# Kernel tuning notes

Hardware: AMD Instinct MI355X
Metric: run time of the kernel (lower is better)

## Reference

```python
import jax, jax.numpy as jnp
import numpy as np

B, D, H, N, K, C = 1024, 256, 512, 100000, 96, 10


def setup_inputs() -> dict:
    key = jax.random.key(0)
    ks = jax.random.split(key, 16)
    s = 0.02
    return {
        "x": jax.random.normal(ks[0], (B, D), jnp.float32),
        "candidate_x": jax.random.normal(ks[1], (N, D), jnp.float32),
        "candidate_labels": jax.random.randint(ks[2], (N,), 0, C, jnp.int32),
        "W_enc": jax.random.normal(ks[3], (D, H), jnp.float32) * s,
        "b_enc": jnp.zeros((H,), jnp.float32),
        "W_key": jax.random.normal(ks[4], (H, H), jnp.float32) * s,
        "b_key": jnp.zeros((H,), jnp.float32),
        "W_val": jax.random.normal(ks[5], (H, H), jnp.float32) * s,
        "b_val": jnp.zeros((H,), jnp.float32),
        "E_label": jax.random.normal(ks[6], (C, H), jnp.float32) * s,
        "W_t1": jax.random.normal(ks[7], (H, H), jnp.float32) * s,
        "b_t1": jnp.zeros((H,), jnp.float32),
        "W_t2": jax.random.normal(ks[8], (H, H), jnp.float32) * s,
    }


def reference(x, candidate_x, candidate_labels, W_enc, b_enc, W_key, b_key,
              W_val, b_val, E_label, W_t1, b_t1, W_t2):
    # Encode queries and candidates
    x_enc = x @ W_enc + b_enc                       # [B, H]
    cand_enc = candidate_x @ W_enc + b_enc          # [N, H]
    x_key = x_enc @ W_key + b_key                   # [B, H]
    cand_keys = cand_enc @ W_key + b_key            # [N, H]

    # Negative euclidean distance via GEMM expansion (compute-efficient cdist)
    q2 = jnp.sum(x_key * x_key, axis=-1, keepdims=True)        # [B, 1]
    c2 = jnp.sum(cand_keys * cand_keys, axis=-1)               # [N]
    d2 = q2 + c2[None, :] - 2.0 * (x_key @ cand_keys.T)        # [B, N]
    sim = -jnp.sqrt(jnp.maximum(d2, 0.0))                      # [B, N]

    # Top-k retrieval
    top_sims, top_idx = jax.lax.top_k(sim, K)                  # [B, K]

    cand_vals = cand_enc @ W_val + b_val                       # [N, H]
    label_emb = E_label[candidate_labels]                      # [N, H]

    ctx_keys = cand_keys[top_idx]                              # [B, K, H]
    ctx_labels = label_emb[top_idx]                            # [B, K, H]
    _ = cand_vals[top_idx]  # gathered values (unused by the original math)

    # Attention over retrieved context (softmax of top-k similarities)
    attn = jax.nn.softmax(top_sims, axis=1)                    # [B, K]

    # Correction MLP T (dropout is identity in eval mode)
    diff = x_key[:, None, :] - ctx_keys                        # [B, K, H]
    t_out = jax.nn.relu(diff @ W_t1 + b_t1) @ W_t2             # [B, K, H]

    ctx_vec = jnp.sum(attn[..., None] * (ctx_labels + t_out), axis=1)  # [B, H]
    return x_enc + ctx_vec
```

## Files before the change

kernel.cpp:

```cpp
#include <hip/hip_runtime.h>
#include <cfloat>
#include <cmath>

#define B_ 1024
#define D_ 256
#define H_ 512
#define N_ 100000
#define K_ 96
#define C_ 10
#define SAMP 4096
#define CAPC 4096
#define RCAP 15

typedef __attribute__((ext_vector_type(8))) short bf16x8;
typedef __attribute__((ext_vector_type(4))) float f32x4;

__device__ __forceinline__ float bf2f(ushort h) {
    union { unsigned u; float f; } v; v.u = ((unsigned)h) << 16; return v.f;
}
__device__ __forceinline__ ushort f2bf(float f) {
    union { float f; unsigned u; } v; v.f = f;
    unsigned u = v.u;
    unsigned r = (u + 0x7fffu + ((u >> 16) & 1u)) >> 16;
    return (ushort)r;
}
__device__ __forceinline__ unsigned f2key(float f) {
    unsigned u = __float_as_uint(f);
    return (u & 0x80000000u) ? ~u : (u | 0x80000000u);
}
__device__ __forceinline__ float d2_of(float acc, float q2, float c2) {
    return fmaxf(fmaf(-2.f, acc, q2 + c2), 0.f);
}

#define GLDS(g, l)                                                            \
    __builtin_amdgcn_global_load_lds(                                         \
        (const __attribute__((address_space(1))) void*)(g),                   \
        (__attribute__((address_space(3))) void*)(l), 16, 0, 0)

#define FENCE() asm volatile("" ::: "memory")

template <int RELU>
__global__ __launch_bounds__(256) void gemm_nn(const float* __restrict__ A,
                                               const float* __restrict__ Bm,
                                               const float* __restrict__ bias,
                                               float* __restrict__ Cm,
                                               int M, int N, int Kd) {
    __shared__ float sA[16][68];
    __shared__ float sB[16][64];
    const int t  = threadIdx.x;
    const int tx = t & 15, ty = t >> 4;
    const int m0 = blockIdx.y * 64;
    const int n0 = blockIdx.x * 64;
    const int lr = t >> 2;
    const int lk = (t & 3) << 2;
    const int bk = t >> 4;
    const int bn = (t & 15) << 2;

    float acc[4][4] = {};
    for (int k0 = 0; k0 < Kd; k0 += 16) {
        float4 av = make_float4(0.f, 0.f, 0.f, 0.f);
        if (m0 + lr < M)
            av = *(const float4*)(A + (size_t)(m0 + lr) * Kd + k0 + lk);
        sA[lk + 0][lr] = av.x; sA[lk + 1][lr] = av.y;
        sA[lk + 2][lr] = av.z; sA[lk + 3][lr] = av.w;
        float4 bv = *(const float4*)(Bm + (size_t)(k0 + bk) * N + n0 + bn);
        *(float4*)&sB[bk][bn] = bv;
        __syncthreads();
#pragma unroll
        for (int kk = 0; kk < 16; ++kk) {
            float4 a4 = *(const float4*)&sA[kk][ty << 2];
            float4 b4 = *(const float4*)&sB[kk][tx << 2];
            float ar[4] = {a4.x, a4.y, a4.z, a4.w};
            float br[4] = {b4.x, b4.y, b4.z, b4.w};
#pragma unroll
            for (int i = 0; i < 4; ++i)
#pragma unroll
                for (int j = 0; j < 4; ++j)
                    acc[i][j] = fmaf(ar[i], br[j], acc[i][j]);
        }
        __syncthreads();
    }
#pragma unroll
    for (int i = 0; i < 4; ++i) {
        int row = m0 + (ty << 2) + i;
        if (row < M) {
            int col = n0 + (tx << 2);
            float b0 = 0.f, b1 = 0.f, b2 = 0.f, b3 = 0.f;
            if (bias) { b0 = bias[col]; b1 = bias[col + 1]; b2 = bias[col + 2]; b3 = bias[col + 3]; }
            float4 o;
            o.x = acc[i][0] + b0; o.y = acc[i][1] + b1;
            o.z = acc[i][2] + b2; o.w = acc[i][3] + b3;
            if (RELU) {
                o.x = fmaxf(o.x, 0.f); o.y = fmaxf(o.y, 0.f);
                o.z = fmaxf(o.z, 0.f); o.w = fmaxf(o.w, 0.f);
            }
            *(float4*)(Cm + (size_t)row * N + col) = o;
        }
    }
}

template <int MODE, int SWZ>
__global__ __launch_bounds__(256) void gemm_nt(const ushort* __restrict__ A,
                                               const ushort* __restrict__ Bv,
                                               const float* __restrict__ bias,
                                               const float* __restrict__ q2v,
                                               const float* __restrict__ c2v,
                                               const float* __restrict__ thrv,
                                               float* __restrict__ candV,
                                               int* __restrict__ candI,
                                               int* __restrict__ cnt,
                                               void* __restrict__ Cout,
                                               int M, int Nlim, int K,
                                               int ldc, int nvalid, int per) {
    int m0, n0;
    if (SWZ == 0) {
        m0 = blockIdx.y * 128; n0 = blockIdx.x * 128;
    } else if (SWZ == 1) {
        int bid = blockIdx.x;
        int xcd = bid & 7, slot = bid >> 3;
        m0 = (slot & 7) * 128;
        n0 = (xcd * per + (slot >> 3)) * 128;
        if (n0 >= nvalid || m0 >= M) return;
    } else {
        int bid = blockIdx.x;
        int xcd = bid & 7, slot = bid >> 3;
        n0 = (slot & 3) * 128;
        m0 = (xcd * per + (slot >> 2)) * 128;
        if (m0 >= M) return;
    }

    __shared__ __align__(16) char smem[32768];
    const int t = threadIdx.x;
    const int lane = t & 63, w = t >> 6;
    const int wm = w & 1, wn = w >> 1;

    f32x4 acc[4][4];
#pragma unroll
    for (int i = 0; i < 4; ++i)
#pragma unroll
        for (int j = 0; j < 4; ++j)
            acc[i][j] = (f32x4){0.f, 0.f, 0.f, 0.f};

    const int la = lane & 15, lk = lane >> 4;
    const int aoff = (wm * 64 + la) * 64 + lk * 16;
    const int boff = (wn * 64 + la) * 64 + lk * 16;
    const int r_ = t >> 2, cc_ = (t & 3);

    auto stage = [&](int k0, int buf) {
#pragma unroll
        for (int q = 0; q < 2; ++q) {
            int r = r_ + q * 64;
            int ar = m0 + r; ar = (ar < M) ? ar : (M - 1);
            GLDS(A + (size_t)ar * K + k0 + cc_ * 8,
                 (char*)smem + buf * 8192 + (q * 256 + t) * 16);
            int br = n0 + r; br = (br < Nlim) ? br : (Nlim - 1);
            GLDS(Bv + (size_t)br * K + k0 + cc_ * 8,
                 (char*)smem + 16384 + buf * 8192 + (q * 256 + t) * 16);
        }
    };

    stage(0, 0);
    int cur = 0;
    for (int k0 = 0; k0 < K; k0 += 32) {
        if (k0 + 32 < K) {
            stage(k0 + 32, cur ^ 1);
            FENCE();
            asm volatile("s_waitcnt vmcnt(4)" ::: "memory");
        } else {
            FENCE();
            asm volatile("s_waitcnt vmcnt(0)" ::: "memory");
        }
        __builtin_amdgcn_s_barrier(); FENCE();

        bf16x8 af[4], bfr[4];
        const char* pA = (const char*)smem + cur * 8192 + aoff;
        const char* pB = (const char*)smem + 16384 + cur * 8192 + boff;
#pragma unroll
        for (int i = 0; i < 4; ++i)
            af[i] = *(const bf16x8*)(pA + i * 1024);
#pragma unroll
        for (int j = 0; j < 4; ++j)
            bfr[j] = *(const bf16x8*)(pB + j * 1024);
#pragma unroll
        for (int i = 0; i < 4; ++i)
#pragma unroll
            for (int j = 0; j < 4; ++j)
                acc[i][j] = __builtin_amdgcn_mfma_f32_16x16x32_bf16(
                    af[i], bfr[j], acc[i][j], 0, 0, 0);

        FENCE();
        asm volatile("s_waitcnt lgkmcnt(0)" ::: "memory");
        __builtin_amdgcn_s_barrier(); FENCE();
        cur ^= 1;
    }

    const int rl = (lane >> 4) * 4, cl = lane & 15;

    if (MODE == 7) {
#pragma unroll
        for (int i = 0; i < 4; ++i) {
#pragma unroll
            for (int v = 0; v < 4; ++v) {
                int gr = m0 + wm * 64 + i * 16 + rl + v;
                float s = 0.f;
#pragma unroll
                for (int j = 0; j < 4; ++j) {
                    int gc = n0 + wn * 64 + j * 16 + cl;
                    float val = acc[i][j][v] + bias[gc];
                    float vb = bf2f(f2bf(val));
                    s = fmaf(vb, vb, s);
                }
                s += __shfl_xor(s, 1);
                s += __shfl_xor(s, 2);
                s += __shfl_xor(s, 4);
                s += __shfl_xor(s, 8);
                if (cl == 0 && gr < M) atomicAdd(&candV[gr], s);
            }
        }
        return;
    }

    if (MODE == 5) {
        float* stV = (float*)smem;
        int*   stI = (int*)(smem + 7680);
        int*   stC = (int*)(smem + 15360);
        for (int r = t; r < 128; r += 256) stC[r] = 0;
        __syncthreads();
#pragma unroll
        for (int i = 0; i < 4; ++i) {
#pragma unroll
            for (int v = 0; v < 4; ++v) {
                int rloc = wm * 64 + i * 16 + rl + v;
                int gr = m0 + rloc;
                float q2b = q2v[gr];
                float th = thrv[gr];
#pragma unroll
                for (int j = 0; j < 4; ++j) {
                    int gc = n0 + wn * 64 + j * 16 + cl;
                    if (gc < nvalid) {
                        float d2 = d2_of(acc[i][j][v], q2b, c2v[gc]);
                        if (d2 <= th) {
                            int p = atomicAdd(&stC[rloc], 1);
                            if (p < RCAP) {
                                stV[rloc * RCAP + p] = d2;
                                stI[rloc * RCAP + p] = gc;
                            } else {
                                int gp = atomicAdd(&cnt[gr], 1);
                                if (gp < CAPC) {
                                    candV[(size_t)gr * CAPC + gp] = d2;
                                    candI[(size_t)gr * CAPC + gp] = gc;
                                }
                            }
                        }
                    }
                }
            }
        }
        __syncthreads();
        for (int r = t; r < 128; r += 256) {
            int n = stC[r]; if (n > RCAP) n = RCAP;
            if (n > 0) {
                int gr = m0 + r;
                int gb = atomicAdd(&cnt[gr], n);
                for (int q = 0; q < n; ++q) {
                    int pos = gb + q;
                    if (pos < CAPC) {
                        candV[(size_t)gr * CAPC + pos] = stV[r * RCAP + q];
                        candI[(size_t)gr * CAPC + pos] = stI[r * RCAP + q];
                    }
                }
            }
        }
        return;
    }

#pragma unroll
    for (int i = 0; i < 4; ++i) {
#pragma unroll
        for (int j = 0; j < 4; ++j) {
            int gc = n0 + wn * 64 + j * 16 + cl;
#pragma unroll
            for (int v = 0; v < 4; ++v) {
                int gr = m0 + wm * 64 + i * 16 + rl + v;
                if (gr < M && gc < nvalid) {
                    float val = acc[i][j][v];
                    if (MODE == 2) {
                        ((float*)Cout)[(size_t)gr * ldc + gc] = val;
                    } else if (MODE == 4) {
                        ((float*)Cout)[(size_t)gr * ldc + gc] = val + bias[gc];
                    } else {
                        if (MODE == 3) val += bias[gc];
                        ((ushort*)Cout)[(size_t)gr * ldc + gc] = f2bf(val);
                    }
                }
            }
        }
    }
}

__global__ __launch_bounds__(256) void thr_select(const float* __restrict__ S,
                                                  int ld,
                                                  const float* __restrict__ q2v,
                                                  const float* __restrict__ c2v,
                                                  float* __restrict__ thrArr) {
    __shared__ unsigned keys[SAMP];
    __shared__ int hist[256];
    __shared__ int sel[2];
    const int b = blockIdx.x, t = threadIdx.x;
    const float q2b = q2v[b];
    for (int i = t; i < SAMP; i += 256)
        keys[i] = ~f2key(d2_of(S[(size_t)b * ld + i], q2b, c2v[i]));
    __syncthreads();
    unsigned prefix = 0, mask = 0;
    int rank = K_;
    for (int shift = 24; shift >= 0; shift -= 8) {
        hist[t & 255] = 0;
        __syncthreads();
        for (int i = t; i < SAMP; i += 256) {
            unsigned k = keys[i];
            if ((k & mask) == prefix) atomicAdd(&hist[(k >> shift) & 255], 1);
        }
        __syncthreads();
        if (t == 0) {
            int r = rank, d = 255;
            for (; d > 0; --d) { int c = hist[d]; if (r - c <= 0) break; r -= c; }
            sel[0] = d; sel[1] = (r < 1) ? 1 : r;
        }
        __syncthreads();
        prefix |= ((unsigned)sel[0]) << shift;
        rank = sel[1];
        mask |= (0xFFu << shift);
        __syncthreads();
    }
    if (t == 0) {
        unsigned key = ~prefix;
        thrArr[b] = __uint_as_float(key & 0x7FFFFFFFu);
    }
}

__global__ __launch_bounds__(256) void final_select(const float* __restrict__ candV,
                                                    const int* __restrict__ candI,
                                                    const int* __restrict__ cnt,
                                                    float* __restrict__ topV,
                                                    int* __restrict__ topI) {
    __shared__ unsigned keys[CAPC];
    __shared__ int hist[256];
    __shared__ int sel[2];
    __shared__ int poscnt, eqcnt;
    const int b = blockIdx.x, t = threadIdx.x;
    int n = cnt[b]; if (n > CAPC) n = CAPC;
    for (int i = t; i < n; i += 256)
        keys[i] = ~f2key(candV[(size_t)b * CAPC + i]);
    __syncthreads();
    unsigned prefix = 0, mask = 0;
    int rank = K_;
    for (int shift = 24; shift >= 0; shift -= 8) {
        hist[t & 255] = 0;
        __syncthreads();
        for (int i = t; i < n; i += 256) {
            unsigned k = keys[i];
            if ((k & mask) == prefix) atomicAdd(&hist[(k >> shift) & 255], 1);
        }
        __syncthreads();
        if (t == 0) {
            int r = rank, d = 255;
            for (; d > 0; --d) { int c = hist[d]; if (r - c <= 0) break; r -= c; }
            sel[0] = d; sel[1] = (r < 1) ? 1 : r;
        }
        __syncthreads();
        prefix |= ((unsigned)sel[0]) << shift;
        rank = sel[1];
        mask |= (0xFFu << shift);
        __syncthreads();
    }
    unsigned kth = prefix;
    if (t == 0) { poscnt = 0; eqcnt = 0; }
    __syncthreads();
    for (int i = t; i < n; i += 256) {
        if (keys[i] > kth) {
            int p = atomicAdd(&poscnt, 1);
            topV[b * K_ + p] = candV[(size_t)b * CAPC + i];
            topI[b * K_ + p] = candI[(size_t)b * CAPC + i];
        }
    }
    __syncthreads();
    int base = poscnt;
    for (int i = t; i < n; i += 256) {
        if (keys[i] == kth) {
            int p = atomicAdd(&eqcnt, 1);
            if (base + p < K_) {
                topV[b * K_ + base + p] = candV[(size_t)b * CAPC + i];
                topI[b * K_ + base + p] = candI[(size_t)b * CAPC + i];
            }
        }
    }
}

__global__ void init_cnt(int* cnt) {
    int i = blockIdx.x * 256 + threadIdx.x;
    if (i < B_) cnt[i] = 0;
}

__global__ void init_f32(float* p, int n) {
    int i = blockIdx.x * 256 + threadIdx.x;
    int stride = gridDim.x * 256;
    for (; i < n; i += stride) p[i] = 0.f;
}

__global__ void conv_f2b(const float* __restrict__ in, ushort* __restrict__ out, int n) {
    int i = (blockIdx.x * 256 + threadIdx.x) * 4;
    int stride = gridDim.x * 256 * 4;
    for (; i < n; i += stride) {
        float4 v = *(const float4*)(in + i);
        ushort4 o;
        o.x = f2bf(v.x); o.y = f2bf(v.y); o.z = f2bf(v.z); o.w = f2bf(v.w);
        *(ushort4*)(out + i) = o;
    }
}

__global__ void conv_f2b_s(const float* __restrict__ in, ushort* __restrict__ out,
                           int ldin) {
    int i = (blockIdx.x * 256 + threadIdx.x) * 4;
    int stride = gridDim.x * 256 * 4;
    int total = B_ * H_;
    for (; i < total; i += stride) {
        int r = i >> 9, c = i & 511;
        float4 v = *(const float4*)(in + (size_t)r * ldin + c);
        ushort4 o;
        o.x = f2bf(v.x); o.y = f2bf(v.y); o.z = f2bf(v.z); o.w = f2bf(v.w);
        *(ushort4*)(out + i) = o;
    }
}

__global__ __launch_bounds__(256) void transpose_f2b(const float* __restrict__ in,
                                                     ushort* __restrict__ out,
                                                     int R, int Cn) {
    __shared__ float tile[32][33];
    int bx = blockIdx.x * 32, by = blockIdx.y * 32;
    int tx = threadIdx.x & 31, ty = threadIdx.x >> 5;
    int x = bx + tx;
#pragma unroll
    for (int dy = 0; dy < 32; dy += 8) {
        int y = by + ty + dy;
        if (x < Cn && y < R) tile[ty + dy][tx] = in[(size_t)y * Cn + x];
    }
    __syncthreads();
    int ox = by + tx;
#pragma unroll
    for (int dy = 0; dy < 32; dy += 8) {
        int oy = bx + ty + dy;
        if (ox < R && oy < Cn) out[(size_t)oy * R + ox] = f2bf(tile[tx][ty + dy]);
    }
}

__global__ void pack_wxx(const float* __restrict__ W_enc,
                         const float* __restrict__ Wc,
                         const float* __restrict__ b_enc,
                         const float* __restrict__ bc,
                         float* __restrict__ Wxx, float* __restrict__ bxx) {
    int i = blockIdx.x * 256 + threadIdx.x;
    if (i < D_ * H_) {
        int k = i >> 9, h = i & 511;
        Wxx[(size_t)k * 1024 + h] = W_enc[i];
        Wxx[(size_t)k * 1024 + 512 + h] = Wc[i];
    }
    if (i < H_) { bxx[i] = b_enc[i]; bxx[512 + i] = bc[i]; }
}

__global__ __launch_bounds__(64) void q2x_k(const ushort* __restrict__ Xb,
                                            const float* __restrict__ Xf,
                                            int ldx,
                                            const float* __restrict__ bc,
                                            float* __restrict__ outv) {
    const int r = blockIdx.x, t = threadIdx.x;
    const ushort* p  = Xb + (size_t)r * H_ + t * 8;
    const float*  xf = Xf + (size_t)r * ldx + t * 8;
    float nrm = 0.f, dot = 0.f;
#pragma unroll
    for (int j = 0; j < 8; ++j) {
        float v = bf2f(p[j]);
        nrm = fmaf(v, v, nrm);
        dot = fmaf(xf[j], bc[t * 8 + j], dot);
    }
    for (int off = 32; off > 0; off >>= 1) {
        nrm += __shfl_down(nrm, off);
        dot += __shfl_down(dot, off);
    }
    if (t == 0) outv[r] = nrm - 2.f * dot;
}

__global__ void bcomb_k(const float* __restrict__ b_enc,
                        const float* __restrict__ W_key,
                        const float* __restrict__ b_key,
                        float* __restrict__ b_comb) {
    int h = blockIdx.x * 256 + threadIdx.x;
    if (h >= H_) return;
    float acc = b_key[h];
    for (int m = 0; m < H_; ++m)
        acc = fmaf(b_enc[m], W_key[(size_t)m * H_ + h], acc);
    b_comb[h] = acc;
}

__global__ void bq_k(const float* __restrict__ bc,
                     const float* __restrict__ W1,
                     float* __restrict__ bq) {
    int h = blockIdx.x * 256 + threadIdx.x;
    if (h >= H_) return;
    float acc = 0.f;
    for (int m = 0; m < H_; ++m)
        acc = fmaf(bc[m], W1[(size_t)m * H_ + h], acc);
    bq[h] = acc;
}

__global__ __launch_bounds__(128) void softmax_k(const float* __restrict__ topVal,
                                                 float* __restrict__ attn) {
    __shared__ float red[128];
    const int b = blockIdx.x, t = threadIdx.x;
    float v = (t < K_) ? -sqrtf(topVal[b * K_ + t]) : -FLT_MAX;
    red[t] = v; __syncthreads();
    for (int s = 64; s > 0; s >>= 1) {
        if (t < s) red[t] = fmaxf(red[t], red[t + s]);
        __syncthreads();
    }
    float m = red[0]; __syncthreads();
    float e = (t < K_) ? expf(v - m) : 0.f;
    red[t] = e; __syncthreads();
    for (int s = 64; s > 0; s >>= 1) {
        if (t < s) red[t] += red[t + s];
        __syncthreads();
    }
    float ssum = red[0];
    if (t < K_) attn[b * K_ + t] = e / ssum;
}

__global__ __launch_bounds__(256) void wsum_q(const float* __restrict__ attn,
                                              const int* __restrict__ topI,
                                              const float* __restrict__ P,
                                              const ushort* __restrict__ Q,
                                              ushort* __restrict__ hw) {
    __shared__ float aw[K_];
    __shared__ int ai[K_];
    const int b = blockIdx.x, t = threadIdx.x;
    if (t < K_) { aw[t] = attn[b * K_ + t]; ai[t] = topI[b * K_ + t]; }
    __syncthreads();
    const float p0 = P[(size_t)b * H_ + 2 * t];
    const float p1 = P[(size_t)b * H_ + 2 * t + 1];
    float a0 = 0.f, a1 = 0.f;
    for (int k = 0; k < K_; ++k) {
        float w = aw[k];
        ushort2 q = *(const ushort2*)(Q + (size_t)ai[k] * H_ + 2 * t);
        a0 = fmaf(w, fmaxf(p0 - bf2f(q.x), 0.f), a0);
        a1 = fmaf(w, fmaxf(p1 - bf2f(q.y), 0.f), a1);
    }
    ushort2 o; o.x = f2bf(a0); o.y = f2bf(a1);
    *(ushort2*)(hw + (size_t)b * H_ + 2 * t) = o;
}

__global__ __launch_bounds__(256) void final_out(const float* __restrict__ attn,
                                                 const int* __restrict__ topI,
                                                 const int* __restrict__ labels,
                                                 const float* __restrict__ E,
                                                 const float* __restrict__ tsum,
                                                 const float* __restrict__ xe,
                                                 int ldxe,
                                                 float* __restrict__ out) {
    const int b = blockIdx.x, t = threadIdx.x;
    float a0 = 0.f, a1 = 0.f;
    for (int k = 0; k < K_; ++k) {
        float w = attn[b * K_ + k];
        int idx = topI[b * K_ + k];
        int lab = labels[idx];
        const float* el = E + (size_t)lab * H_;
        a0 = fmaf(w, el[t], a0);
        a1 = fmaf(w, el[t + 256], a1);
    }
    out[(size_t)b * H_ + t] =
        xe[(size_t)b * ldxe + t] + a0 + tsum[(size_t)b * H_ + t];
    out[(size_t)b * H_ + t + 256] =
        xe[(size_t)b * ldxe + t + 256] + a1 + tsum[(size_t)b * H_ + t + 256];
}

extern "C" void kernel_launch(void* const* d_in, const int* in_sizes, int n_in,
                              void* d_out, int out_size, void* d_ws, size_t ws_size,
                              hipStream_t stream) {
    const float* x      = (const float*)d_in[0];
    const float* cx     = (const float*)d_in[1];
    const int*   labels = (const int*)d_in[2];
    const float* W_enc  = (const float*)d_in[3];
    const float* b_enc  = (const float*)d_in[4];
    const float* W_key  = (const float*)d_in[5];
    const float* b_key  = (const float*)d_in[6];
    const float* E_label = (const float*)d_in[9];
    const float* W_t1   = (const float*)d_in[10];
    const float* b_t1   = (const float*)d_in[11];
    const float* W_t2   = (const float*)d_in[12];
    float* out = (float*)d_out;

    char* base = (char*)d_ws;
    size_t off = 0;
    auto take = [&](size_t n) -> char* {
        char* p = base + off;
        off = (off + n + 255) & ~(size_t)255;
        return p;
    };
    float*  Wc    = (float*)take((size_t)D_ * H_ * 4);
    float*  bc    = (float*)take((size_t)H_ * 4);
    float*  Wxx   = (float*)take((size_t)D_ * 1024 * 4);
    float*  bxx   = (float*)take((size_t)1024 * 4);
    ushort* WcT   = (ushort*)take((size_t)H_ * D_ * 2);
    ushort* Wcb   = (ushort*)take((size_t)D_ * H_ * 2);
    float*  Wq    = (float*)take((size_t)D_ * H_ * 4);
    ushort* WqT   = (ushort*)take((size_t)H_ * D_ * 2);
    float*  bq    = (float*)take((size_t)H_ * 4);
    ushort* Wt1T  = (ushort*)take((size_t)H_ * H_ * 2);
    ushort* Wt2T  = (ushort*)take((size_t)H_ * H_ * 2);
    float*  xekk  = (float*)take((size_t)B_ * 1024 * 4);
    ushort* xkb   = (ushort*)take((size_t)B_ * H_ * 2);
    ushort* xprojb= (ushort*)take((size_t)B_ * D_ * 2);
    float*  q2x   = (float*)take((size_t)B_ * 4);
    float*  c2    = (float*)take((size_t)N_ * 4);
    float*  topV  = (float*)take((size_t)B_ * K_ * 4);
    int*    topI  = (int*)take((size_t)B_ * K_ * 4);
    float*  thr   = (float*)take((size_t)B_ * 4);
    float*  attn  = (float*)take((size_t)B_ * K_ * 4);
    int*    cnt   = (int*)take((size_t)B_ * 4);
    float*  candV = (float*)take((size_t)B_ * CAPC * 4);
    int*    candI = (int*)take((size_t)B_ * CAPC * 4);
    ushort* hwAll = (ushort*)take((size_t)B_ * H_ * 2);
    float*  tsum  = (float*)take((size_t)B_ * H_ * 4);
    float*  Pbuf  = (float*)take((size_t)B_ * H_ * 4);
    ushort* Qb    = (ushort*)take((size_t)N_ * H_ * 2);
    char*   big   = base + off;

    ushort* cxb = (ushort*)big;
    float* simSmall = (float*)candV;

    const float* xeView = xekk;
    const float* xkView = xekk + 512;

    {
        dim3 g(H_ / 64, D_ / 64);
        gemm_nn<0><<<g, 256, 0, stream>>>(W_enc, W_key, nullptr, Wc, D_, H_, H_);
        bcomb_k<<<(H_ + 255) / 256, 256, 0, stream>>>(b_enc, W_key, b_key, bc);
        gemm_nn<0><<<g, 256, 0, stream>>>(Wc, W_t1, nullptr, Wq, D_, H_, H_);
        bq_k<<<(H_ + 255) / 256, 256, 0, stream>>>(bc, W_t1, bq);
        pack_wxx<<<(D_ * H_ + 255) / 256, 256, 0, stream>>>(W_enc, Wc, b_enc,
                                                            bc, Wxx, bxx);
        dim3 gt1((H_ + 31) / 32, (D_ + 31) / 32);
        transpose_f2b<<<gt1, 256, 0, stream>>>(Wc, WcT, D_, H_);
        transpose_f2b<<<gt1, 256, 0, stream>>>(Wq, WqT, D_, H_);
        conv_f2b<<<128, 256, 0, stream>>>(Wc, Wcb, D_ * H_);
        dim3 gt2((H_ + 31) / 32, (H_ + 31) / 32);
        transpose_f2b<<<gt2, 256, 0, stream>>>(W_t1, Wt1T, H_, H_);
        transpose_f2b<<<gt2, 256, 0, stream>>>(W_t2, Wt2T, H_, H_);
    }
    {
        dim3 gx(1024 / 64, B_ / 64);
        gemm_nn<0><<<gx, 256, 0, stream>>>(x, Wxx, bxx, xekk, B_, 1024, D_);
        conv_f2b_s<<<1024, 256, 0, stream>>>(xkView, xkb, 1024);
        conv_f2b<<<2048, 256, 0, stream>>>(cx, cxb, N_ * D_);
        dim3 gp(D_ / 128, B_ / 128);
        gemm_nt<0, 0><<<gp, 256, 0, stream>>>(
            xkb, Wcb, nullptr, nullptr, nullptr, nullptr, nullptr, nullptr,
            nullptr, xprojb, B_, D_, H_, D_, D_, 0);
        q2x_k<<<B_, 64, 0, stream>>>(xkb, xkView, 1024, bc, q2x);
        dim3 gq(H_ / 128, B_ / 128);
        gemm_nt<4, 0><<<gq, 256, 0, stream>>>(
            xkb, Wt1T, b_t1, nullptr, nullptr, nullptr, nullptr, nullptr,
            nullptr, Pbuf, B_, H_, H_, H_, H_, 0);
    }
    init_f32<<<128, 256, 0, stream>>>(c2, N_);
    {
        int mt = (N_ + 127) / 128;
        int mper = (mt + 7) / 8;
        gemm_nt<7, 2><<<8 * mper * 4, 256, 0, stream>>>(
            cxb, WcT, bc, nullptr, nullptr, nullptr, c2, nullptr, nullptr,
            nullptr, N_, H_, D_, H_, H_, mper);
    }
    {
        int nper = (SAMP / 128 + 7) / 8;
        gemm_nt<2, 1><<<64 * nper, 256, 0, stream>>>(
            xprojb, cxb, nullptr, nullptr, nullptr, nullptr, nullptr, nullptr,
            nullptr, simSmall, B_, N_, D_, SAMP, SAMP, nper);
        thr_select<<<B_, 256, 0, stream>>>(simSmall, SAMP, q2x, c2, thr);
    }
    init_cnt<<<(B_ + 255) / 256, 256, 0, stream>>>(cnt);
    {
        int NT = (N_ + 127) / 128;
        int nper = (NT + 7) / 8;
        gemm_nt<5, 1><<<64 * nper, 256, 0, stream>>>(
            xprojb, cxb, nullptr, q2x, c2, thr, candV, candI, cnt,
            nullptr, B_, N_, D_, 0, N_, nper);
    }
    {
        int mt = (N_ + 127) / 128;
        int mper = (mt + 7) / 8;
        gemm_nt<3, 2><<<8 * mper * 4, 256, 0, stream>>>(
            cxb, WqT, bq, nullptr, nullptr, nullptr, nullptr, nullptr,
            nullptr, Qb, N_, H_, D_, H_, H_, mper);
    }
    final_select<<<B_, 256, 0, stream>>>(candV, candI, cnt, topV, topI);
    softmax_k<<<B_, 128, 0, stream>>>(topV, attn);

    wsum_q<<<B_, 256, 0, stream>>>(attn, topI, Pbuf, Qb, hwAll);
    {
        dim3 g(H_ / 128, B_ / 128);
        gemm_nt<2, 0><<<g, 256, 0, stream>>>(
            hwAll, Wt2T, nullptr, nullptr, nullptr, nullptr, nullptr, nullptr,
            nullptr, tsum, B_, H_, H_, H_, H_, 0);
    }
    final_out<<<B_, 256, 0, stream>>>(attn, topI, labels, E_label, tsum,
                                      xeView, 1024, out);
}
```

Before: 827.0 us.

## Fold query-side projections into one widened packed GEMM from x

The query-side GEMMs (xkb·Wc for xproj, xkb·Wt1 for P) are precomputed as weight products (Wq, G2 = Wc·Wcᵀ) and appended as extra columns to the packed encoder weight, so one GEMM on x yields x_enc, x_key, P and xproj. This removes two dependent GEMM launches, the bf16 conversion of x_key, and the Pbuf buffer. It adds a small Wc·Wcᵀ GEMM and a wider main GEMM, and rounding changes because the products now go through fp32 weight folding instead of bf16 activations.

Result: no change. 837.8 us (+1.3%).

```diff
diff --git a/kernel.cpp b/kernel.cpp
--- a/kernel.cpp
+++ b/kernel.cpp
@@ -11,6 +11,7 @@
 #define SAMP 4096
 #define CAPC 4096
 #define RCAP 15
+#define WXN 1792
 
 typedef __attribute__((ext_vector_type(8))) short bf16x8;
 typedef __attribute__((ext_vector_type(4))) float f32x4;
@@ -286,8 +287,6 @@
                     float val = acc[i][j][v];
                     if (MODE == 2) {
                         ((float*)Cout)[(size_t)gr * ldc + gc] = val;
-                    } else if (MODE == 4) {
-                        ((float*)Cout)[(size_t)gr * ldc + gc] = val + bias[gc];
                     } else {
                         if (MODE == 3) val += bias[gc];
                         ((ushort*)Cout)[(size_t)gr * ldc + gc] = f2bf(val);
@@ -418,13 +417,13 @@
     }
 }
 
-__global__ void conv_f2b_s(const float* __restrict__ in, ushort* __restrict__ out,
-                           int ldin) {
+__global__ void conv_rows(const float* __restrict__ in, ushort* __restrict__ out,
+                          int R, int C, int ldin) {
     int i = (blockIdx.x * 256 + threadIdx.x) * 4;
     int stride = gridDim.x * 256 * 4;
-    int total = B_ * H_;
+    int total = R * C;
     for (; i < total; i += stride) {
-        int r = i >> 9, c = i & 511;
+        int r = i / C, c = i % C;
         float4 v = *(const float4*)(in + (size_t)r * ldin + c);
         ushort4 o;
         o.x = f2bf(v.x); o.y = f2bf(v.y); o.z = f2bf(v.z); o.w = f2bf(v.w);
@@ -455,32 +454,48 @@
 
 __global__ void pack_wxx(const float* __restrict__ W_enc,
                          const float* __restrict__ Wc,
+                         const float* __restrict__ Wq,
+                         const float* __restrict__ G2,
                          const float* __restrict__ b_enc,
                          const float* __restrict__ bc,
+                         const float* __restrict__ bq,
+                         const float* __restrict__ b_t1,
+                         const float* __restrict__ bcw,
                          float* __restrict__ Wxx, float* __restrict__ bxx) {
     int i = blockIdx.x * 256 + threadIdx.x;
-    if (i < D_ * H_) {
-        int k = i >> 9, h = i & 511;
-        Wxx[(size_t)k * 1024 + h] = W_enc[i];
-        Wxx[(size_t)k * 1024 + 512 + h] = Wc[i];
-    }
-    if (i < H_) { bxx[i] = b_enc[i]; bxx[512 + i] = bc[i]; }
-}
-
-__global__ __launch_bounds__(64) void q2x_k(const ushort* __restrict__ Xb,
-                                            const float* __restrict__ Xf,
+    int total = D_ * WXN;
+    if (i < total) {
+        int k = i / WXN, c = i % WXN;
+        float v;
+        if (c < 512)       v = W_enc[(size_t)k * 512 + c];
+        else if (c < 1024) v = Wc[(size_t)k * 512 + (c - 512)];
+        else if (c < 1536) v = Wq[(size_t)k * 512 + (c - 1024)];
+        else               v = G2[(size_t)k * 256 + (c - 1536)];
+        Wxx[(size_t)k * WXN + c] = v;
+    }
+    if (i < WXN) {
+        float b;
+        if (i < 512)       b = b_enc[i];
+        else if (i < 1024) b = bc[i - 512];
+        else if (i < 1536) b = bq[i - 1024] + b_t1[i - 1024];
+        else               b = bcw[i - 1536];
+        bxx[i] = b;
+    }
+}
+
+__global__ __launch_bounds__(64) void q2x_k(const float* __restrict__ Xf,
                                             int ldx,
                                             const float* __restrict__ bc,
                                             float* __restrict__ outv) {
     const int r = blockIdx.x, t = threadIdx.x;
-    const ushort* p  = Xb + (size_t)r * H_ + t * 8;
-    const float*  xf = Xf + (size_t)r * ldx + t * 8;
+    const float* xf = Xf + (size_t)r * ldx + t * 8;
     float nrm = 0.f, dot = 0.f;
 #pragma unroll
     for (int j = 0; j < 8; ++j) {
-        float v = bf2f(p[j]);
+        float raw = xf[j];
+        float v = bf2f(f2bf(raw));
         nrm = fmaf(v, v, nrm);
-        dot = fmaf(xf[j], bc[t * 8 + j], dot);
+        dot = fmaf(raw, bc[t * 8 + j], dot);
     }
     for (int off = 32; off > 0; off >>= 1) {
         nrm += __shfl_down(nrm, off);
@@ -512,6 +527,17 @@
     bq[h] = acc;
 }
 
+__global__ void bcw_k(const float* __restrict__ bc,
+                      const float* __restrict__ Wc,
+                      float* __restrict__ outv) {
+    int d = blockIdx.x * 256 + threadIdx.x;
+    if (d >= D_) return;
+    float acc = 0.f;
+    for (int h = 0; h < H_; ++h)
+        acc = fmaf(bc[h], Wc[(size_t)d * H_ + h], acc);
+    outv[d] = acc;
+}
+
 __global__ __launch_bounds__(128) void softmax_k(const float* __restrict__ topVal,
                                                  float* __restrict__ attn) {
     __shared__ float red[128];
@@ -536,6 +562,7 @@
 __global__ __launch_bounds__(256) void wsum_q(const float* __restrict__ attn,
                                               const int* __restrict__ topI,
                                               const float* __restrict__ P,
+                                              int ldp,
                                               const ushort* __restrict__ Q,
                                               ushort* __restrict__ hw) {
     __shared__ float aw[K_];
@@ -543,8 +570,8 @@
     const int b = blockIdx.x, t = threadIdx.x;
     if (t < K_) { aw[t] = attn[b * K_ + t]; ai[t] = topI[b * K_ + t]; }
     __syncthreads();
-    const float p0 = P[(size_t)b * H_ + 2 * t];
-    const float p1 = P[(size_t)b * H_ + 2 * t + 1];
+    const float p0 = P[(size_t)b * ldp + 2 * t];
+    const float p1 = P[(size_t)b * ldp + 2 * t + 1];
     float a0 = 0.f, a1 = 0.f;
     for (int k = 0; k < K_; ++k) {
         float w = aw[k];
@@ -605,17 +632,17 @@
     };
     float*  Wc    = (float*)take((size_t)D_ * H_ * 4);
     float*  bc    = (float*)take((size_t)H_ * 4);
-    float*  Wxx   = (float*)take((size_t)D_ * 1024 * 4);
-    float*  bxx   = (float*)take((size_t)1024 * 4);
+    float*  Wq    = (float*)take((size_t)D_ * H_ * 4);
+    float*  bq    = (float*)take((size_t)H_ * 4);
+    float*  G2    = (float*)take((size_t)D_ * D_ * 4);
+    float*  bcw   = (float*)take((size_t)D_ * 4);
+    float*  Wxx   = (float*)take((size_t)D_ * WXN * 4);
+    float*  bxx   = (float*)take((size_t)WXN * 4);
     ushort* WcT   = (ushort*)take((size_t)H_ * D_ * 2);
     ushort* Wcb   = (ushort*)take((size_t)D_ * H_ * 2);
-    float*  Wq    = (float*)take((size_t)D_ * H_ * 4);
     ushort* WqT   = (ushort*)take((size_t)H_ * D_ * 2);
-    float*  bq    = (float*)take((size_t)H_ * 4);
-    ushort* Wt1T  = (ushort*)take((size_t)H_ * H_ * 2);
     ushort* Wt2T  = (ushort*)take((size_t)H_ * H_ * 2);
-    float*  xekk  = (float*)take((size_t)B_ * 1024 * 4);
-    ushort* xkb   = (ushort*)take((size_t)B_ * H_ * 2);
+    float*  xekk  = (float*)take((size_t)B_ * WXN * 4);
     ushort* xprojb= (ushort*)take((size_t)B_ * D_ * 2);
     float*  q2x   = (float*)take((size_t)B_ * 4);
     float*  c2    = (float*)take((size_t)N_ * 4);
@@ -628,15 +655,16 @@
     int*    candI = (int*)take((size_t)B_ * CAPC * 4);
     ushort* hwAll = (ushort*)take((size_t)B_ * H_ * 2);
     float*  tsum  = (float*)take((size_t)B_ * H_ * 4);
-    float*  Pbuf  = (float*)take((size_t)B_ * H_ * 4);
     ushort* Qb    = (ushort*)take((size_t)N_ * H_ * 2);
     char*   big   = base + off;
 
     ushort* cxb = (ushort*)big;
     float* simSmall = (float*)candV;
 
-    const float* xeView = xekk;
-    const float* xkView = xekk + 512;
+    const float* xeView    = xekk;
+    const float* xkView    = xekk + 512;
+    const float* pView     = xekk + 1024;
+    const float* xprojView = xekk + 1536;
 
     {
         dim3 g(H_ / 64, D_ / 64);
@@ -644,30 +672,28 @@
         bcomb_k<<<(H_ + 255) / 256, 256, 0, stream>>>(b_enc, W_key, b_key, bc);
         gemm_nn<0><<<g, 256, 0, stream>>>(Wc, W_t1, nullptr, Wq, D_, H_, H_);
         bq_k<<<(H_ + 255) / 256, 256, 0, stream>>>(bc, W_t1, bq);
-        pack_wxx<<<(D_ * H_ + 255) / 256, 256, 0, stream>>>(W_enc, Wc, b_enc,
-                                                            bc, Wxx, bxx);
+        bcw_k<<<(D_ + 255) / 256, 256, 0, stream>>>(bc, Wc, bcw);
+        conv_f2b<<<128, 256, 0, stream>>>(Wc, Wcb, D_ * H_);
+        {
+            dim3 gg(D_ / 128, D_ / 128);
+            gemm_nt<2, 0><<<gg, 256, 0, stream>>>(
+                Wcb, Wcb, nullptr, nullptr, nullptr, nullptr, nullptr, nullptr,
+                nullptr, G2, D_, D_, H_, D_, D_, 0);
+        }
         dim3 gt1((H_ + 31) / 32, (D_ + 31) / 32);
         transpose_f2b<<<gt1, 256, 0, stream>>>(Wc, WcT, D_, H_);
         transpose_f2b<<<gt1, 256, 0, stream>>>(Wq, WqT, D_, H_);
-        conv_f2b<<<128, 256, 0, stream>>>(Wc, Wcb, D_ * H_);
         dim3 gt2((H_ + 31) / 32, (H_ + 31) / 32);
-        transpose_f2b<<<gt2, 256, 0, stream>>>(W_t1, Wt1T, H_, H_);
         transpose_f2b<<<gt2, 256, 0, stream>>>(W_t2, Wt2T, H_, H_);
+        pack_wxx<<<(D_ * WXN + 255) / 256, 256, 0, stream>>>(
+            W_enc, Wc, Wq, G2, b_enc, bc, bq, b_t1, bcw, Wxx, bxx);
     }
     {
-        dim3 gx(1024 / 64, B_ / 64);
-        gemm_nn<0><<<gx, 256, 0, stream>>>(x, Wxx, bxx, xekk, B_, 1024, D_);
-        conv_f2b_s<<<1024, 256, 0, stream>>>(xkView, xkb, 1024);
+        dim3 gx(WXN / 64, B_ / 64);
+        gemm_nn<0><<<gx, 256, 0, stream>>>(x, Wxx, bxx, xekk, B_, WXN, D_);
+        conv_rows<<<256, 256, 0, stream>>>(xprojView, xprojb, B_, D_, WXN);
         conv_f2b<<<2048, 256, 0, stream>>>(cx, cxb, N_ * D_);
-        dim3 gp(D_ / 128, B_ / 128);
-        gemm_nt<0, 0><<<gp, 256, 0, stream>>>(
-            xkb, Wcb, nullptr, nullptr, nullptr, nullptr, nullptr, nullptr,
-            nullptr, xprojb, B_, D_, H_, D_, D_, 0);
-        q2x_k<<<B_, 64, 0, stream>>>(xkb, xkView, 1024, bc, q2x);
-        dim3 gq(H_ / 128, B_ / 128);
-        gemm_nt<4, 0><<<gq, 256, 0, stream>>>(
-            xkb, Wt1T, b_t1, nullptr, nullptr, nullptr, nullptr, nullptr,
-            nullptr, Pbuf, B_, H_, H_, H_, H_, 0);
+        q2x_k<<<B_, 64, 0, stream>>>(xkView, WXN, bc, q2x);
     }
     init_f32<<<128, 256, 0, stream>>>(c2, N_);
     {
@@ -702,7 +728,7 @@
     final_select<<<B_, 256, 0, stream>>>(candV, candI, cnt, topV, topI);
     softmax_k<<<B_, 128, 0, stream>>>(topV, attn);
 
-    wsum_q<<<B_, 256, 0, stream>>>(attn, topI, Pbuf, Qb, hwAll);
+    wsum_q<<<B_, 256, 0, stream>>>(attn, topI, pView, WXN, Qb, hwAll);
     {
         dim3 g(H_ / 128, B_ / 128);
         gemm_nt<2, 0><<<g, 256, 0, stream>>>(
@@ -710,5 +736,5 @@
             nullptr, tsum, B_, H_, H_, H_, H_, 0);
     }
     final_out<<<B_, 256, 0, stream>>>(attn, topI, labels, E_label, tsum,
-                                      xeView, 1024, out);
-}
+                                      xeView, WXN, out);
+}
```
